# Optimization experiments

Hardware: AMD Instinct MI355X
Metric: run time of the kernel (lower is better)

The kernel has to match this reference:

```python
import jax, jax.numpy as jnp
import numpy as np

HEADS = 8
HEAD_CH = 64
CH = 512
INNER = HEADS * HEAD_CH  # 512
BETA = 0.9

def setup_inputs() -> dict:
    key = jax.random.key(0)
    ks = jax.random.split(key, 8)
    B, N = 4, 16384
    s = 1.0 / np.sqrt(CH)
    return {
        "x": jax.random.normal(ks[0], (B, N, CH), jnp.float32),
        "mask": jnp.ones((B, N), dtype=bool),
        "Wh": jax.random.uniform(ks[1], (CH, INNER), jnp.float32, -s, s),
        "bh": jax.random.uniform(ks[2], (INNER,), jnp.float32, -s, s),
        "Wk": jax.random.uniform(ks[3], (CH, INNER), jnp.float32, -s, s),
        "Wv": jax.random.uniform(ks[4], (CH, INNER), jnp.float32, -s, s),
        "ln_g": jnp.ones((INNER,), jnp.float32),
        "ln_b": jnp.zeros((INNER,), jnp.float32),
        "Wo": jax.random.uniform(ks[5], (INNER, INNER), jnp.float32, -s, s),
        "bo": jax.random.uniform(ks[6], (INNER,), jnp.float32, -s, s),
    }

def _layernorm(x, g, b, eps=1e-5):
    mu = jnp.mean(x, axis=-1, keepdims=True)
    var = jnp.var(x, axis=-1, keepdims=True)
    return (x - mu) * jax.lax.rsqrt(var + eps) * g + b

def reference(x, mask, Wh, bh, Wk, Wv, ln_g, ln_b, Wo, bo):
    B, N, _ = x.shape
    h = x @ Wh + bh                                        # [B,N,INNER]
    k = jax.nn.sigmoid(x @ Wk).reshape(B, N, HEAD_CH, HEADS)
    q = k  # qk_shared=True
    v = (x @ Wv).reshape(B, N, HEAD_CH, HEADS)
    v = jnp.where(mask[:, :, None, None], v, 0.0)
    kv = jnp.einsum('bndh,bnmh->bdmh', k, v)               # [B,d,d,H]
    num = jnp.einsum('bndh,bdmh->bnmh', q, kv)             # [B,N,d,H]
    k_sum = jnp.sum(k, axis=1)                             # [B,d,H]
    den = jnp.einsum('bndh,bdh->bnh', q, k_sum)[:, :, None, :]
    out = (num / (den + 1e-6)).reshape(B, N, INNER)
    out = _layernorm(out, ln_g, ln_b) * (h + BETA)
    return jax.nn.relu(out @ Wo + bo)
```

## Files before the change

kernel.cpp:

```cpp
#include <hip/hip_runtime.h>
#include <stdint.h>


#define HEADS 8
#define HD 64
#define NSEQ 16384
#define ROWS 65536
#define NT 8

typedef __attribute__((ext_vector_type(8))) short short8;
typedef __attribute__((ext_vector_type(4))) float f32x4;
typedef unsigned short u16;
typedef unsigned int u32;
typedef u32 __attribute__((address_space(1))) gu32;
typedef u32 __attribute__((address_space(3))) lu32;

__device__ __forceinline__ u16 f2bf(float f) {
    u32 u = __builtin_bit_cast(u32, f);
    u += 0x7fffu + ((u >> 16) & 1u);
    return (u16)(u >> 16);
}
__device__ __forceinline__ float bf2f(u16 h) { return __builtin_bit_cast(float, (u32)h << 16); }
__device__ __forceinline__ float blo(u32 u) { return __builtin_bit_cast(float, u << 16); }
__device__ __forceinline__ float bhi(u32 u) { return __builtin_bit_cast(float, u & 0xffff0000u); }
__device__ __forceinline__ u32 pk(float a, float b) { return (u32)f2bf(a) | ((u32)f2bf(b) << 16); }

__device__ __forceinline__ void gld16(const void* g, void* l) {
    __builtin_amdgcn_global_load_lds((const gu32*)g, (lu32*)l, 16, 0, 0);
}

__device__ __forceinline__ void bar() {
    asm volatile("" ::: "memory");
    __builtin_amdgcn_s_barrier();
    asm volatile("" ::: "memory");
}

__global__ __launch_bounds__(256) void cvt_x(const float* __restrict__ x, u16* __restrict__ xb) {
    size_t i = ((size_t)blockIdx.x * 256 + threadIdx.x) * 8;
    float4 a = *(const float4*)(x + i);
    float4 c = *(const float4*)(x + i + 4);
    uint4 o;
    o.x = pk(a.x, a.y);
    o.y = pk(a.z, a.w);
    o.z = pk(c.x, c.y);
    o.w = pk(c.z, c.w);
    *(uint4*)(xb + i) = o;
}

__global__ __launch_bounds__(256) void cvt_w(const float* __restrict__ Wh, const float* __restrict__ Wk,
                                             const float* __restrict__ Wv, const float* __restrict__ Wo,
                                             u16* __restrict__ WT, u16* __restrict__ WoT) {
    int gid = blockIdx.x * 256 + threadIdx.x;
    if (gid < 1536 * 512) {
        int c = gid & 511, j = gid >> 9;
        const float* src = (j < 512) ? Wh : ((j < 1024) ? Wk : Wv);
        int col = j & 511;
        WT[gid] = f2bf(src[c * 512 + col]);
    } else {
        int g2 = gid - 1536 * 512;
        int c = g2 & 511, j = g2 >> 9;
        WoT[g2] = f2bf(Wo[c * 512 + j]);
    }
}

__device__ __forceinline__ void stage_half(const u16* __restrict__ gp, int gr, int kt,
                                           u16* sm, int hb, int tid, int wave) {
#pragma unroll
    for (int it = 0; it < 2; ++it) {
        int lc = it * 512 + tid;
        int r = lc >> 3;
        int cg = (lc & 7) ^ (r & 7);
        gld16(gp + (size_t)(gr + r) * 512 + kt * 64 + cg * 8, &sm[hb + (it * 512 + wave * 64) * 8]);
    }
}

__device__ __forceinline__ void gemm256(const u16* __restrict__ Ag, const u16* __restrict__ Bg,
                                        int m0, int j0, int tid, u16* sm, f32x4 (&acc)[8][4]) {
    int wave = tid >> 6, lane = tid & 63, q = lane >> 4, ln = lane & 15;
    int wm = (wave >> 2) * 128, wn = (wave & 3) * 64;
#pragma unroll
    for (int a1 = 0; a1 < 8; a1++)
#pragma unroll
        for (int a2 = 0; a2 < 4; a2++) acc[a1][a2] = (f32x4){0.f, 0.f, 0.f, 0.f};

    stage_half(Bg, j0, 0, sm, 16384, tid, wave);
    stage_half(Bg, j0 + 128, 0, sm, 24576, tid, wave);
    stage_half(Ag, m0, 0, sm, 0, tid, wave);
    stage_half(Ag, m0 + 128, 0, sm, 8192, tid, wave);
    stage_half(Bg, j0, 1, sm, 32768 + 16384, tid, wave);
    stage_half(Bg, j0 + 128, 1, sm, 32768 + 24576, tid, wave);
    stage_half(Ag, m0, 1, sm, 32768 + 0, tid, wave);
    asm volatile("s_waitcnt vmcnt(6)" ::: "memory");
    bar();

#pragma unroll
    for (int t = 0; t < NT; ++t) {
        const int bufC = (t & 1) * 32768;
        const int bufN = ((t & 1) ^ 1) * 32768;
        short8 a0[4][2], a1[4][2], b0[2][2], b1[2][2];

#pragma unroll
        for (int f = 0; f < 4; ++f) {
            int mr = wm + f * 16 + ln;
#pragma unroll
            for (int kk = 0; kk < 2; ++kk) {
                int cs = (kk * 4 + q) ^ (mr & 7);
                a0[f][kk] = *(const short8*)&sm[bufC + mr * 64 + cs * 8];
            }
        }
#pragma unroll
        for (int f = 0; f < 2; ++f) {
            int nr = wn + f * 16 + ln;
#pragma unroll
            for (int kk = 0; kk < 2; ++kk) {
                int cs = (kk * 4 + q) ^ (nr & 7);
                b0[f][kk] = *(const short8*)&sm[bufC + 16384 + nr * 64 + cs * 8];
            }
        }
        if (t + 1 < NT) stage_half(Ag, m0 + 128, t + 1, sm, bufN + 8192, tid, wave);
        bar();
        __builtin_amdgcn_s_setprio(1);
#pragma unroll
        for (int f = 0; f < 4; ++f)
#pragma unroll
            for (int g = 0; g < 2; ++g)
#pragma unroll
                for (int kk = 0; kk < 2; ++kk)
                    acc[f][g] = __builtin_amdgcn_mfma_f32_16x16x32_bf16(a0[f][kk], b0[g][kk], acc[f][g], 0, 0, 0);
        __builtin_amdgcn_s_setprio(0);
        bar();

#pragma unroll
        for (int f = 0; f < 2; ++f) {
            int nr = wn + (2 + f) * 16 + ln;
#pragma unroll
            for (int kk = 0; kk < 2; ++kk) {
                int cs = (kk * 4 + q) ^ (nr & 7);
                b1[f][kk] = *(const short8*)&sm[bufC + 16384 + nr * 64 + cs * 8];
            }
        }
        bar();
        __builtin_amdgcn_s_setprio(1);
#pragma unroll
        for (int f = 0; f < 4; ++f)
#pragma unroll
            for (int g = 0; g < 2; ++g)
#pragma unroll
                for (int kk = 0; kk < 2; ++kk)
                    acc[f][2 + g] = __builtin_amdgcn_mfma_f32_16x16x32_bf16(a0[f][kk], b1[g][kk], acc[f][2 + g], 0, 0, 0);
        __builtin_amdgcn_s_setprio(0);
        bar();

#pragma unroll
        for (int f = 0; f < 4; ++f) {
            int mr = wm + (4 + f) * 16 + ln;
#pragma unroll
            for (int kk = 0; kk < 2; ++kk) {
                int cs = (kk * 4 + q) ^ (mr & 7);
                a1[f][kk] = *(const short8*)&sm[bufC + mr * 64 + cs * 8];
            }
        }
        if (t + 2 < NT) stage_half(Bg, j0, t + 2, sm, bufC + 16384, tid, wave);
        bar();
        __builtin_amdgcn_s_setprio(1);
#pragma unroll
        for (int f = 0; f < 4; ++f)
#pragma unroll
            for (int g = 0; g < 2; ++g)
#pragma unroll
                for (int kk = 0; kk < 2; ++kk)
                    acc[4 + f][2 + g] = __builtin_amdgcn_mfma_f32_16x16x32_bf16(a1[f][kk], b1[g][kk], acc[4 + f][2 + g], 0, 0, 0);
        __builtin_amdgcn_s_setprio(0);
        bar();

        if (t + 2 < NT) {
            stage_half(Bg, j0 + 128, t + 2, sm, bufC + 24576, tid, wave);
            stage_half(Ag, m0, t + 2, sm, bufC + 0, tid, wave);
        }
        bar();
        __builtin_amdgcn_s_setprio(1);
#pragma unroll
        for (int f = 0; f < 4; ++f)
#pragma unroll
            for (int g = 0; g < 2; ++g)
#pragma unroll
                for (int kk = 0; kk < 2; ++kk)
                    acc[4 + f][g] = __builtin_amdgcn_mfma_f32_16x16x32_bf16(a1[f][kk], b0[g][kk], acc[4 + f][g], 0, 0, 0);
        __builtin_amdgcn_s_setprio(0);
        if (t + 2 < NT)
            asm volatile("s_waitcnt vmcnt(6)" ::: "memory");
        else
            asm volatile("s_waitcnt vmcnt(0)" ::: "memory");
        bar();
    }
}

#define EST 264
__global__ __launch_bounds__(512) void gemm_proj(const u16* __restrict__ A, const u16* __restrict__ BT,
                                                 const float* __restrict__ bh, u16* __restrict__ hbuf,
                                                 u16* __restrict__ kr, u16* __restrict__ vr) {
    __shared__ u16 sm[65536];
    int tid = threadIdx.x;
    int hw = blockIdx.y * 6 + blockIdx.x;
    int wg = (hw & 7) * 192 + (hw >> 3);
    int bx = wg % 6, by = wg / 6;
    int j0 = bx * 256, m0 = by * 256;
    f32x4 acc[8][4];
    gemm256(A, BT, m0, j0, tid, sm, acc);

    int wave = tid >> 6, lane = tid & 63, q = lane >> 4, ln = lane & 15;
    int wn = (wave & 3) * 64;
    int region = j0 >> 9;
    int b = m0 >> 14;
    int nl0 = m0 & 16383;
    int d0b = (region == 1) ? ((j0 - 512) >> 3) : ((j0 - 1024) >> 3);

#pragma unroll
    for (int ph = 0; ph < 2; ++ph) {
        if ((wave >> 2) == ph) {
#pragma unroll
            for (int mf = 0; mf < 8; ++mf) {
                int lrow = mf * 16 + q * 4;
#pragma unroll
                for (int nf = 0; nf < 4; ++nf) {
                    int cl = wn + nf * 16 + ln;
                    f32x4 a = acc[mf][nf];
                    if (region == 0) {
                        float bias = bh[j0 + cl];
#pragma unroll
                        for (int r = 0; r < 4; ++r) sm[(lrow + r) * EST + cl] = f2bf(a[r] + bias);
                    } else {
                        int pos = (cl & 7) * 32 + (cl >> 3);
                        if (region == 1) {
#pragma unroll
                            for (int r = 0; r < 4; ++r) {
                                float s = 1.f / (1.f + __expf(-a[r]));
                                sm[(lrow + r) * EST + pos] = f2bf(s);
                            }
                        } else {
#pragma unroll
                            for (int r = 0; r < 4; ++r) sm[(lrow + r) * EST + pos] = f2bf(a[r]);
                        }
                    }
                }
            }
        }
        __syncthreads();
#pragma unroll
        for (int it = 0; it < 8; ++it) {
            int e = it * 512 + tid;
            int row = e >> 5, c = e & 31;
            uint4 u = *(const uint4*)&sm[row * EST + c * 8];
            if (region == 0) {
                *(uint4*)(hbuf + (size_t)(m0 + ph * 128 + row) * 512 + j0 + c * 8) = u;
            } else {
                u16* dst = (region == 1) ? kr : vr;
                int hh = c >> 2, dl = (c & 3) * 8;
                *(uint4*)(dst + ((size_t)(b * HEADS + hh) * NSEQ + nl0 + ph * 128 + row) * 64 + d0b + dl) = u;
            }
        }
        __syncthreads();
    }
}

__global__ __launch_bounds__(256) void kv_part(const u16* __restrict__ kr, const u16* __restrict__ vr,
                                               float* __restrict__ part) {
    __shared__ float kf[64 * 64];
    __shared__ float vf[64 * 64];
    int tid = threadIdx.x;
    int bh = blockIdx.x >> 5, s = blockIdx.x & 31;
    int d0 = (tid >> 4) * 4, m0 = (tid & 15) * 4;
    float acc[4][4] = {};
    float ks[4] = {0.f, 0.f, 0.f, 0.f};
    size_t kb = ((size_t)bh * NSEQ + (size_t)s * 512) * 64;
    for (int c = 0; c < 8; c++) {
        __syncthreads();
#pragma unroll
        for (int it = 0; it < 2; it++) {
            int e = it * 256 + tid;
            uint4 uk = *(const uint4*)(kr + kb + c * 4096 + e * 8);
            uint4 uv = *(const uint4*)(vr + kb + c * 4096 + e * 8);
            float4 k1 = {blo(uk.x), bhi(uk.x), blo(uk.y), bhi(uk.y)};
            float4 k2 = {blo(uk.z), bhi(uk.z), blo(uk.w), bhi(uk.w)};
            float4 v1 = {blo(uv.x), bhi(uv.x), blo(uv.y), bhi(uv.y)};
            float4 v2 = {blo(uv.z), bhi(uv.z), blo(uv.w), bhi(uv.w)};
            *(float4*)&kf[e * 8] = k1;
            *(float4*)&kf[e * 8 + 4] = k2;
            *(float4*)&vf[e * 8] = v1;
            *(float4*)&vf[e * 8 + 4] = v2;
        }
        __syncthreads();
        for (int n = 0; n < 64; n++) {
            float4 k4 = *(const float4*)&kf[n * 64 + d0];
            float4 v4 = *(const float4*)&vf[n * 64 + m0];
            float ka[4] = {k4.x, k4.y, k4.z, k4.w};
            float va[4] = {v4.x, v4.y, v4.z, v4.w};
#pragma unroll
            for (int di = 0; di < 4; di++)
#pragma unroll
                for (int mi = 0; mi < 4; mi++) acc[di][mi] += ka[di] * va[mi];
            if ((tid & 15) == 0) {
#pragma unroll
                for (int di = 0; di < 4; di++) ks[di] += ka[di];
            }
        }
    }
    float* po = part + (size_t)blockIdx.x * 4160;
#pragma unroll
    for (int di = 0; di < 4; di++) {
        float4 w = {acc[di][0], acc[di][1], acc[di][2], acc[di][3]};
        *(float4*)&po[(d0 + di) * 64 + m0] = w;
    }
    if ((tid & 15) == 0) {
#pragma unroll
        for (int di = 0; di < 4; di++) po[4096 + d0 + di] = ks[di];
    }
}

__global__ __launch_bounds__(256) void kv_reduce(const float* __restrict__ part, u16* __restrict__ kvT,
                                                 float* __restrict__ ksum) {
    int gid = blockIdx.x * 256 + threadIdx.x;
    int bh = gid >> 12, rem = gid & 4095;
    int d = rem >> 6, m = rem & 63;
    float sum = 0.f;
    for (int s2 = 0; s2 < 32; s2++) sum += part[((size_t)bh * 32 + s2) * 4160 + rem];
    kvT[((size_t)bh * 64 + m) * 64 + d] = f2bf(sum);
    if (gid < 2048) {
        int bh2 = gid >> 6, dd = gid & 63;
        float s3 = 0.f;
        for (int s2 = 0; s2 < 32; s2++) s3 += part[((size_t)bh2 * 32 + s2) * 4160 + 4096 + dd];
        ksum[gid] = s3;
    }
}

#define OSTR 520
__global__ __launch_bounds__(256) void attn_ln(const u16* __restrict__ kr, const u16* __restrict__ kvT,
                                               const float* __restrict__ ksum, const u16* __restrict__ hbuf,
                                               const float* __restrict__ lng, const float* __restrict__ lnb,
                                               u16* __restrict__ tbuf) {
    __shared__ u16 ot[64 * OSTR];
    __shared__ float den[64 * 8];
    __shared__ float murs[64 * 2];
    __shared__ float gw[512], bw[512];
    int tid = threadIdx.x, wave = tid >> 6, lane = tid & 63, q = lane >> 4, ln = lane & 15;
    int n0 = blockIdx.x * 64;
    int b = n0 >> 14;
    int nl0 = n0 & 16383;

    for (int i = tid; i < 512; i += 256) { gw[i] = lng[i]; bw[i] = lnb[i]; }

#pragma unroll
    for (int rep = 0; rep < 2; rep++) {
        int idx = rep * 256 + tid;
        int nl = idx >> 3, hh = idx & 7;
        const u16* krow = kr + ((size_t)(b * HEADS + hh) * NSEQ + nl0 + nl) * 64;
        const float* kss = ksum + (b * HEADS + hh) * 64;
        float sum = 0.f;
#pragma unroll
        for (int dc = 0; dc < 8; dc++) {
            uint4 u = *(const uint4*)(krow + dc * 8);
            float4 s1 = *(const float4*)(kss + dc * 8);
            float4 s2 = *(const float4*)(kss + dc * 8 + 4);
            sum += blo(u.x) * s1.x + bhi(u.x) * s1.y + blo(u.y) * s1.z + bhi(u.y) * s1.w
                 + blo(u.z) * s2.x + bhi(u.z) * s2.y + blo(u.w) * s2.z + bhi(u.w) * s2.w;
        }
        den[nl * 8 + hh] = sum;
    }
    __syncthreads();

    int nrow = nl0 + wave * 16 + ln;
    float s1a[4] = {0.f, 0.f, 0.f, 0.f}, s2a[4] = {0.f, 0.f, 0.f, 0.f};
#pragma unroll
    for (int g = 0; g < 2; g++) {
        f32x4 acc[4][4];
#pragma unroll
        for (int a1 = 0; a1 < 4; a1++)
#pragma unroll
            for (int a2 = 0; a2 < 4; a2++) acc[a1][a2] = (f32x4){0.f, 0.f, 0.f, 0.f};
#pragma unroll
        for (int hg = 0; hg < 4; hg++) {
            int hh = g * 4 + hg;
            const u16* kbase = kr + ((size_t)(b * HEADS + hh) * NSEQ + nrow) * 64;
            const u16* vb = kvT + (size_t)(b * HEADS + hh) * 4096;
#pragma unroll
            for (int kk = 0; kk < 2; kk++) {
                short8 af = *(const short8*)(kbase + kk * 32 + q * 8);
#pragma unroll
                for (int mb = 0; mb < 4; mb++) {
                    short8 bf2 = *(const short8*)(vb + (size_t)(mb * 16 + ln) * 64 + kk * 32 + q * 8);
                    acc[hg][mb] = __builtin_amdgcn_mfma_f32_16x16x32_bf16(af, bf2, acc[hg][mb], 0, 0, 0);
                }
            }
        }
#pragma unroll
        for (int r = 0; r < 4; r++) {
            int nl = wave * 16 + q * 4 + r;
#pragma unroll
            for (int hg = 0; hg < 4; hg++) {
                int hh = g * 4 + hg;
                float rin = 1.f / (den[nl * 8 + hh] + 1e-6f);
#pragma unroll
                for (int mb = 0; mb < 4; mb++) {
                    float oo = acc[hg][mb][r] * rin;
                    s1a[r] += oo;
                    s2a[r] += oo * oo;
                    ot[nl * OSTR + (mb * 16 + ln) * 8 + hh] = f2bf(oo);
                }
            }
        }
    }
#pragma unroll
    for (int r = 0; r < 4; r++) {
        float a = s1a[r], c = s2a[r];
#pragma unroll
        for (int off = 1; off < 16; off <<= 1) {
            a += __shfl_xor(a, off);
            c += __shfl_xor(c, off);
        }
        float mu = a * (1.f / 512.f);
        float var = c * (1.f / 512.f) - mu * mu;
        float rs = rsqrtf(var + 1e-5f);
        if (ln == 0) {
            int nl = wave * 16 + q * 4 + r;
            murs[nl * 2] = mu;
            murs[nl * 2 + 1] = rs;
        }
    }
    __syncthreads();

#pragma unroll
    for (int it = 0; it < 16; it++) {
        int e = it * 256 + tid;
        int row = e >> 6, c = e & 63;
        uint4 o8 = *(const uint4*)&ot[row * OSTR + c * 8];
        uint4 hu = *(const uint4*)(hbuf + (size_t)(n0 + row) * 512 + c * 8);
        float mu = murs[row * 2], rs = murs[row * 2 + 1];
        float4 g1 = *(const float4*)&gw[c * 8];
        float4 g2 = *(const float4*)&gw[c * 8 + 4];
        float4 b1 = *(const float4*)&bw[c * 8];
        float4 b2 = *(const float4*)&bw[c * 8 + 4];
        float v0 = ((blo(o8.x) - mu) * rs * g1.x + b1.x) * (blo(hu.x) + 0.9f);
        float v1 = ((bhi(o8.x) - mu) * rs * g1.y + b1.y) * (bhi(hu.x) + 0.9f);
        float v2 = ((blo(o8.y) - mu) * rs * g1.z + b1.z) * (blo(hu.y) + 0.9f);
        float v3 = ((bhi(o8.y) - mu) * rs * g1.w + b1.w) * (bhi(hu.y) + 0.9f);
        float v4 = ((blo(o8.z) - mu) * rs * g2.x + b2.x) * (blo(hu.z) + 0.9f);
        float v5 = ((bhi(o8.z) - mu) * rs * g2.y + b2.y) * (bhi(hu.z) + 0.9f);
        float v6 = ((blo(o8.w) - mu) * rs * g2.z + b2.z) * (blo(hu.w) + 0.9f);
        float v7 = ((bhi(o8.w) - mu) * rs * g2.w + b2.w) * (bhi(hu.w) + 0.9f);
        uint4 res;
        res.x = pk(v0, v1);
        res.y = pk(v2, v3);
        res.z = pk(v4, v5);
        res.w = pk(v6, v7);
        *(uint4*)(tbuf + (size_t)(n0 + row) * 512 + c * 8) = res;
    }
}

__global__ __launch_bounds__(512) void gemm_out(const u16* __restrict__ A, const u16* __restrict__ BT,
                                                const float* __restrict__ bo, float* __restrict__ out) {
    __shared__ u16 sm[65536];
    int tid = threadIdx.x;
    int hw = blockIdx.y * 2 + blockIdx.x;
    int wg = (hw & 7) * 64 + (hw >> 3);
    int bx = wg & 1, by = wg >> 1;
    int j0 = bx * 256, m0 = by * 256;
    f32x4 acc[8][4];
    gemm256(A, BT, m0, j0, tid, sm, acc);

    int wave = tid >> 6, lane = tid & 63, q = lane >> 4, ln = lane & 15;
    int wm = (wave >> 2) * 128, wn = (wave & 3) * 64;
#pragma unroll
    for (int mf = 0; mf < 8; ++mf) {
        int rowb = m0 + wm + mf * 16 + q * 4;
#pragma unroll
        for (int nf = 0; nf < 4; ++nf) {
            int col = j0 + wn + nf * 16 + ln;
            float bias = bo[col];
            f32x4 a = acc[mf][nf];
#pragma unroll
            for (int r = 0; r < 4; ++r)
                out[(size_t)(rowb + r) * 512 + col] = fmaxf(a[r] + bias, 0.f);
        }
    }
}

extern "C" void kernel_launch(void* const* d_in, const int* in_sizes, int n_in,
                              void* d_out, int out_size, void* d_ws, size_t ws_size,
                              hipStream_t stream) {
    (void)in_sizes; (void)n_in; (void)out_size; (void)ws_size;
    const float* x   = (const float*)d_in[0];
    const float* Wh  = (const float*)d_in[2];
    const float* bh  = (const float*)d_in[3];
    const float* Wk  = (const float*)d_in[4];
    const float* Wv  = (const float*)d_in[5];
    const float* lng = (const float*)d_in[6];
    const float* lnb = (const float*)d_in[7];
    const float* Wo  = (const float*)d_in[8];
    const float* bo  = (const float*)d_in[9];
    float* out = (float*)d_out;
    char* ws = (char*)d_ws;

    u16*   xb   = (u16*)(ws);
    u16*   WT   = (u16*)(ws + 67108864);
    u16*   WoT  = (u16*)(ws + 68681728);
    u16*   hbuf = (u16*)(ws + 69206016);
    u16*   kr   = (u16*)(ws + 136314880);
    u16*   vr   = (u16*)(ws + 203423744);
    float* part = (float*)(ws + 270532608);
    u16*   kvT  = (u16*)(ws + 287571968);
    float* ksum = (float*)(ws + 287834112);
    u16*   tbuf = xb;

    hipLaunchKernelGGL(cvt_x,     dim3(16384),   dim3(256), 0, stream, x, xb);
    hipLaunchKernelGGL(cvt_w,     dim3(4096),    dim3(256), 0, stream, Wh, Wk, Wv, Wo, WT, WoT);
    hipLaunchKernelGGL(gemm_proj, dim3(6, 256),  dim3(512), 0, stream, xb, WT, bh, hbuf, kr, vr);
    hipLaunchKernelGGL(kv_part,   dim3(1024),    dim3(256), 0, stream, kr, vr, part);
    hipLaunchKernelGGL(kv_reduce, dim3(512),     dim3(256), 0, stream, part, kvT, ksum);
    hipLaunchKernelGGL(attn_ln,   dim3(1024),    dim3(256), 0, stream, kr, kvT, ksum, hbuf, lng, lnb, tbuf);
    hipLaunchKernelGGL(gemm_out,  dim3(2, 256),  dim3(512), 0, stream, tbuf, WoT, bo, out);
}
```

Before: 640.8 us.

## Fuse denominator into attention MFMA loop, use inline LDS reads, contiguous k/v layout

The attention/LayerNorm kernel no longer runs a separate pass that reloads k rows to compute the denominator. Each lane now forms a partial dot product from the k fragment it already holds for the MFMA and reduces it with shuffles. The projection GEMM reads LDS through inline-asm ds_read_b128 with explicit lgkmcnt fences, which pins the instruction schedule. The k/v weight columns are permuted on the host-side conversion so the epilogue writes contiguous columns instead of scattering, at the cost of extra shuffles and tighter scheduling constraints.

```diff
diff --git a/kernel.cpp b/kernel.cpp
--- a/kernel.cpp
+++ b/kernel.cpp
@@ -14,6 +14,7 @@
 typedef unsigned int u32;
 typedef u32 __attribute__((address_space(1))) gu32;
 typedef u32 __attribute__((address_space(3))) lu32;
+typedef u16 __attribute__((address_space(3))) lu16;
 
 __device__ __forceinline__ u16 f2bf(float f) {
     u32 u = __builtin_bit_cast(u32, f);
@@ -33,6 +34,16 @@
     asm volatile("" ::: "memory");
     __builtin_amdgcn_s_barrier();
     asm volatile("" ::: "memory");
+}
+
+__device__ __forceinline__ short8 ldsr(const lu16* p) {
+    short8 d;
+    asm volatile("ds_read_b128 %0, %1" : "=&v"(d) : "v"(p));
+    return d;
+}
+__device__ __forceinline__ void lgkm0_fence() {
+    asm volatile("s_waitcnt lgkmcnt(0)" ::: "memory");
+    __builtin_amdgcn_sched_barrier(0);
 }
 
 __global__ __launch_bounds__(256) void cvt_x(const float* __restrict__ x, u16* __restrict__ xb) {
@@ -53,9 +64,15 @@
     int gid = blockIdx.x * 256 + threadIdx.x;
     if (gid < 1536 * 512) {
         int c = gid & 511, j = gid >> 9;
-        const float* src = (j < 512) ? Wh : ((j < 1024) ? Wk : Wv);
-        int col = j & 511;
-        WT[gid] = f2bf(src[c * 512 + col]);
+        float val;
+        if (j < 512) {
+            val = Wh[c * 512 + j];
+        } else {
+            int jj = j & 511;
+            int col = (jj & 63) * 8 + (jj >> 6);
+            val = (j < 1024) ? Wk[c * 512 + col] : Wv[c * 512 + col];
+        }
+        WT[gid] = f2bf(val);
     } else {
         int g2 = gid - 1536 * 512;
         int c = g2 & 511, j = g2 >> 9;
@@ -78,6 +95,7 @@
                                         int m0, int j0, int tid, u16* sm, f32x4 (&acc)[8][4]) {
     int wave = tid >> 6, lane = tid & 63, q = lane >> 4, ln = lane & 15;
     int wm = (wave >> 2) * 128, wn = (wave & 3) * 64;
+    const lu16* ls = (const lu16*)sm;
 #pragma unroll
     for (int a1 = 0; a1 < 8; a1++)
 #pragma unroll
@@ -105,7 +123,7 @@
 #pragma unroll
             for (int kk = 0; kk < 2; ++kk) {
                 int cs = (kk * 4 + q) ^ (mr & 7);
-                a0[f][kk] = *(const short8*)&sm[bufC + mr * 64 + cs * 8];
+                a0[f][kk] = ldsr(ls + bufC + mr * 64 + cs * 8);
             }
         }
 #pragma unroll
@@ -114,9 +132,10 @@
 #pragma unroll
             for (int kk = 0; kk < 2; ++kk) {
                 int cs = (kk * 4 + q) ^ (nr & 7);
-                b0[f][kk] = *(const short8*)&sm[bufC + 16384 + nr * 64 + cs * 8];
-            }
-        }
+                b0[f][kk] = ldsr(ls + bufC + 16384 + nr * 64 + cs * 8);
+            }
+        }
+        lgkm0_fence();
         if (t + 1 < NT) stage_half(Ag, m0 + 128, t + 1, sm, bufN + 8192, tid, wave);
         bar();
         __builtin_amdgcn_s_setprio(1);
@@ -136,9 +155,10 @@
 #pragma unroll
             for (int kk = 0; kk < 2; ++kk) {
                 int cs = (kk * 4 + q) ^ (nr & 7);
-                b1[f][kk] = *(const short8*)&sm[bufC + 16384 + nr * 64 + cs * 8];
-            }
-        }
+                b1[f][kk] = ldsr(ls + bufC + 16384 + nr * 64 + cs * 8);
+            }
+        }
+        lgkm0_fence();
         bar();
         __builtin_amdgcn_s_setprio(1);
 #pragma unroll
@@ -157,9 +177,10 @@
 #pragma unroll
             for (int kk = 0; kk < 2; ++kk) {
                 int cs = (kk * 4 + q) ^ (mr & 7);
-                a1[f][kk] = *(const short8*)&sm[bufC + mr * 64 + cs * 8];
-            }
-        }
+                a1[f][kk] = ldsr(ls + bufC + mr * 64 + cs * 8);
+            }
+        }
+        lgkm0_fence();
         if (t + 2 < NT) stage_half(Bg, j0, t + 2, sm, bufC + 16384, tid, wave);
         bar();
         __builtin_amdgcn_s_setprio(1);
@@ -213,7 +234,6 @@
     int region = j0 >> 9;
     int b = m0 >> 14;
     int nl0 = m0 & 16383;
-    int d0b = (region == 1) ? ((j0 - 512) >> 3) : ((j0 - 1024) >> 3);
 
 #pragma unroll
     for (int ph = 0; ph < 2; ++ph) {
@@ -229,18 +249,15 @@
                         float bias = bh[j0 + cl];
 #pragma unroll
                         for (int r = 0; r < 4; ++r) sm[(lrow + r) * EST + cl] = f2bf(a[r] + bias);
+                    } else if (region == 1) {
+#pragma unroll
+                        for (int r = 0; r < 4; ++r) {
+                            float s = 1.f / (1.f + __expf(-a[r]));
+                            sm[(lrow + r) * EST + cl] = f2bf(s);
+                        }
                     } else {
-                        int pos = (cl & 7) * 32 + (cl >> 3);
-                        if (region == 1) {
-#pragma unroll
-                            for (int r = 0; r < 4; ++r) {
-                                float s = 1.f / (1.f + __expf(-a[r]));
-                                sm[(lrow + r) * EST + pos] = f2bf(s);
-                            }
-                        } else {
-#pragma unroll
-                            for (int r = 0; r < 4; ++r) sm[(lrow + r) * EST + pos] = f2bf(a[r]);
-                        }
+#pragma unroll
+                        for (int r = 0; r < 4; ++r) sm[(lrow + r) * EST + cl] = f2bf(a[r]);
                     }
                 }
             }
@@ -255,8 +272,9 @@
                 *(uint4*)(hbuf + (size_t)(m0 + ph * 128 + row) * 512 + j0 + c * 8) = u;
             } else {
                 u16* dst = (region == 1) ? kr : vr;
-                int hh = c >> 2, dl = (c & 3) * 8;
-                *(uint4*)(dst + ((size_t)(b * HEADS + hh) * NSEQ + nl0 + ph * 128 + row) * 64 + d0b + dl) = u;
+                int jj = j0 - ((region == 1) ? 512 : 1024) + c * 8;
+                int hh = jj >> 6, dl = jj & 63;
+                *(uint4*)(dst + ((size_t)(b * HEADS + hh) * NSEQ + nl0 + ph * 128 + row) * 64 + dl) = u;
             }
         }
         __syncthreads();
@@ -339,7 +357,6 @@
                                                const float* __restrict__ lng, const float* __restrict__ lnb,
                                                u16* __restrict__ tbuf) {
     __shared__ u16 ot[64 * OSTR];
-    __shared__ float den[64 * 8];
     __shared__ float murs[64 * 2];
     __shared__ float gw[512], bw[512];
     int tid = threadIdx.x, wave = tid >> 6, lane = tid & 63, q = lane >> 4, ln = lane & 15;
@@ -349,30 +366,12 @@
 
     for (int i = tid; i < 512; i += 256) { gw[i] = lng[i]; bw[i] = lnb[i]; }
 
-#pragma unroll
-    for (int rep = 0; rep < 2; rep++) {
-        int idx = rep * 256 + tid;
-        int nl = idx >> 3, hh = idx & 7;
-        const u16* krow = kr + ((size_t)(b * HEADS + hh) * NSEQ + nl0 + nl) * 64;
-        const float* kss = ksum + (b * HEADS + hh) * 64;
-        float sum = 0.f;
-#pragma unroll
-        for (int dc = 0; dc < 8; dc++) {
-            uint4 u = *(const uint4*)(krow + dc * 8);
-            float4 s1 = *(const float4*)(kss + dc * 8);
-            float4 s2 = *(const float4*)(kss + dc * 8 + 4);
-            sum += blo(u.x) * s1.x + bhi(u.x) * s1.y + blo(u.y) * s1.z + bhi(u.y) * s1.w
-                 + blo(u.z) * s2.x + bhi(u.z) * s2.y + blo(u.w) * s2.z + bhi(u.w) * s2.w;
-        }
-        den[nl * 8 + hh] = sum;
-    }
-    __syncthreads();
-
     int nrow = nl0 + wave * 16 + ln;
     float s1a[4] = {0.f, 0.f, 0.f, 0.f}, s2a[4] = {0.f, 0.f, 0.f, 0.f};
 #pragma unroll
     for (int g = 0; g < 2; g++) {
         f32x4 acc[4][4];
+        float dpg[4];
 #pragma unroll
         for (int a1 = 0; a1 < 4; a1++)
 #pragma unroll
@@ -382,15 +381,27 @@
             int hh = g * 4 + hg;
             const u16* kbase = kr + ((size_t)(b * HEADS + hh) * NSEQ + nrow) * 64;
             const u16* vb = kvT + (size_t)(b * HEADS + hh) * 4096;
+            const float* kss = ksum + (b * HEADS + hh) * 64;
+            float dp = 0.f;
 #pragma unroll
             for (int kk = 0; kk < 2; kk++) {
                 short8 af = *(const short8*)(kbase + kk * 32 + q * 8);
+                const float* sv = kss + kk * 32 + q * 8;
+                float4 s1 = *(const float4*)(sv);
+                float4 s2 = *(const float4*)(sv + 4);
+                dp += bf2f((u16)af[0]) * s1.x + bf2f((u16)af[1]) * s1.y
+                    + bf2f((u16)af[2]) * s1.z + bf2f((u16)af[3]) * s1.w
+                    + bf2f((u16)af[4]) * s2.x + bf2f((u16)af[5]) * s2.y
+                    + bf2f((u16)af[6]) * s2.z + bf2f((u16)af[7]) * s2.w;
 #pragma unroll
                 for (int mb = 0; mb < 4; mb++) {
-                    short8 bf2 = *(const short8*)(vb + (size_t)(mb * 16 + ln) * 64 + kk * 32 + q * 8);
-                    acc[hg][mb] = __builtin_amdgcn_mfma_f32_16x16x32_bf16(af, bf2, acc[hg][mb], 0, 0, 0);
+                    short8 bf2r = *(const short8*)(vb + (size_t)(mb * 16 + ln) * 64 + kk * 32 + q * 8);
+                    acc[hg][mb] = __builtin_amdgcn_mfma_f32_16x16x32_bf16(af, bf2r, acc[hg][mb], 0, 0, 0);
                 }
             }
+            dp += __shfl_xor(dp, 16);
+            dp += __shfl_xor(dp, 32);
+            dpg[hg] = dp;
         }
 #pragma unroll
         for (int r = 0; r < 4; r++) {
@@ -398,7 +409,8 @@
 #pragma unroll
             for (int hg = 0; hg < 4; hg++) {
                 int hh = g * 4 + hg;
-                float rin = 1.f / (den[nl * 8 + hh] + 1e-6f);
+                float dn = __shfl(dpg[hg], q * 4 + r, 16);
+                float rin = 1.f / (dn + 1e-6f);
 #pragma unroll
                 for (int mb = 0; mb < 4; mb++) {
                     float oo = acc[hg][mb][r] * rin;
```

New measurement: 790.7 us. 23.4% more time.
